# Optimization experiments

Hardware: AMD Instinct MI355X
Metric: run time of the kernel (lower is better)

Reference implementation:

```python
import jax, jax.numpy as jnp
import numpy as np

B, S, NQ, H, HD = 2, 4096, 576, 32, 128
HID = H * HD  # 4096


def setup_inputs() -> dict:
    key = jax.random.key(0)
    ks = jax.random.split(key, 7)
    sc = 0.02
    return {
        "hidden_states": jax.random.normal(ks[0], (B, S, HID), jnp.float32),
        "by_pass_hidden_states": jax.random.normal(ks[1], (B, NQ, HID), jnp.float32),
        "attention_mask": jnp.zeros((B, 1, S, NQ), jnp.float32),
        "Wq": jax.random.normal(ks[2], (HID, HID), jnp.float32) * sc,
        "Wk": jax.random.normal(ks[3], (HID, HID), jnp.float32) * sc,
        "Wv": jax.random.normal(ks[4], (HID, HID), jnp.float32) * sc,
        "Wo": jax.random.normal(ks[5], (HID, HID), jnp.float32) * sc,
    }


def reference(hidden_states, by_pass_hidden_states, attention_mask, Wq, Wk, Wv, Wo):
    b, s, _ = hidden_states.shape
    nq = by_pass_hidden_states.shape[1]
    # projections (nn.Linear applies x @ W.T); reshape to (b, heads, len, head_dim)
    q = (hidden_states @ Wq.T).reshape(b, s, H, HD).transpose(0, 2, 1, 3)
    k = (by_pass_hidden_states @ Wk.T).reshape(b, nq, H, HD).transpose(0, 2, 1, 3)
    v = (by_pass_hidden_states @ Wv.T).reshape(b, nq, H, HD).transpose(0, 2, 1, 3)
    # eager QK^T -> mask -> fp32 softmax -> V
    scores = jnp.einsum("bhsd,bhqd->bhsq", q, k) / jnp.sqrt(jnp.float32(HD))
    scores = scores + attention_mask  # (b,1,s,nq) broadcast over heads
    attn = jax.nn.softmax(scores.astype(jnp.float32), axis=-1).astype(q.dtype)
    out = jnp.einsum("bhsq,bhqd->bhsd", attn, v)
    out = out.transpose(0, 2, 1, 3).reshape(b, s, HID)
    return out @ Wo.T
```

## Files before the change

kernel.cpp:

```cpp
#include <hip/hip_runtime.h>
#include <stdint.h>

#define Bn   2
#define Sn   4096
#define NQn  576
#define Hn   32
#define HDn  128
#define HIDn 4096

typedef unsigned short bfu;
typedef short short8 __attribute__((ext_vector_type(8)));
typedef float f32x4 __attribute__((ext_vector_type(4)));

__device__ __forceinline__ bfu f2b(float f) {
  uint32_t x = __builtin_bit_cast(uint32_t, f);
  return (bfu)((x + 0x7fffu + ((x >> 16) & 1u)) >> 16);
}

__device__ __forceinline__ void gload16(const void* g, void* l) {
  __builtin_amdgcn_global_load_lds(
      (const __attribute__((address_space(1))) uint32_t*)g,
      (__attribute__((address_space(3))) uint32_t*)l, 16, 0, 0);
}

__device__ __forceinline__ void cast8(const float* s, bfu* d, long i) {
  const float4* in4 = (const float4*)s;
  float4 a = in4[2 * i], c = in4[2 * i + 1];
  short8 v;
  v[0] = (short)f2b(a.x); v[1] = (short)f2b(a.y);
  v[2] = (short)f2b(a.z); v[3] = (short)f2b(a.w);
  v[4] = (short)f2b(c.x); v[5] = (short)f2b(c.y);
  v[6] = (short)f2b(c.z); v[7] = (short)f2b(c.w);
  ((short8*)d)[i] = v;
}

__global__ void cast_f32_bf16(const float* __restrict__ in, bfu* __restrict__ out,
                              int n8) {
  long i = (long)blockIdx.x * 256 + threadIdx.x;
  if (i >= n8) return;
  cast8(in, out, i);
}

__global__ void cast5(const float* s0, bfu* d0, int n0, const float* s1, bfu* d1,
                      int n1, const float* s2, bfu* d2, int n2, const float* s3,
                      bfu* d3, int n3, const float* s4, bfu* d4, int n4) {
  long gid = (long)blockIdx.x * 256 + threadIdx.x;
  if (gid < n0) { cast8(s0, d0, gid); return; }
  gid -= n0;
  if (gid < n1) { cast8(s1, d1, gid); return; }
  gid -= n1;
  if (gid < n2) { cast8(s2, d2, gid); return; }
  gid -= n2;
  if (gid < n3) { cast8(s3, d3, gid); return; }
  gid -= n3;
  if (gid < n4) cast8(s4, d4, gid);
}

template <int WRITE_BF16>
__global__ __launch_bounds__(512, 2)
void gemm_bt256(const bfu* __restrict__ A, const bfu* __restrict__ Bm,
                void* __restrict__ Cout, int M, int N, int K) {
  __shared__ __align__(16) bfu Asm[2][256 * 64];
  __shared__ __align__(16) bfu Bsm[2][256 * 64];
  const int tid = threadIdx.x;
  const int wave = tid >> 6, lane = tid & 63;
  const int lr = lane & 15, kq = lane >> 4;
  const int wm = wave >> 2, wn = wave & 3;
  const long m0 = (long)blockIdx.y * 256, n0 = (long)blockIdx.x * 256;
  const int NT = K >> 6;

  const int c0j = tid >> 3, c0c = tid & 7;
  const int c1j = (512 + tid) >> 3, c1c = tid & 7;
  const bfu* aSrc0 = A + (m0 + c0j) * (long)K + ((c0c ^ (c0j & 7)) * 8);
  const bfu* aSrc1 = A + (m0 + c1j) * (long)K + ((c1c ^ (c1j & 7)) * 8);
  const bfu* bSrc0 = Bm + (n0 + c0j) * (long)K + ((c0c ^ (c0j & 7)) * 8);
  const bfu* bSrc1 = Bm + (n0 + c1j) * (long)K + ((c1c ^ (c1j & 7)) * 8);

  auto stageA = [&](int t, int buf, int half) {
    long koff = (long)t * 64 + (long)half * 128 * K;
    gload16(aSrc0 + koff, &Asm[buf][half * 8192 + (wave * 64) * 8]);
    gload16(aSrc1 + koff, &Asm[buf][half * 8192 + (512 + wave * 64) * 8]);
  };
  auto stageB = [&](int t, int buf, int half) {
    long koff = (long)t * 64 + (long)half * 128 * K;
    gload16(bSrc0 + koff, &Bsm[buf][half * 8192 + (wave * 64) * 8]);
    gload16(bSrc1 + koff, &Bsm[buf][half * 8192 + (512 + wave * 64) * 8]);
  };
  auto ldsA = [&](int buf, int mf, int ks) -> short8 {
    int row = (mf >> 2) * 128 + wm * 64 + (mf & 3) * 16 + lr;
    int off = (row * 128 + ks * 64 + kq * 16) ^ ((row & 7) << 4);
    return *(const short8*)((const char*)Asm[buf] + off);
  };
  auto ldsB = [&](int buf, int nf, int ks) -> short8 {
    int row = (nf >> 1) * 128 + wn * 32 + (nf & 1) * 16 + lr;
    int off = (row * 128 + ks * 64 + kq * 16) ^ ((row & 7) << 4);
    return *(const short8*)((const char*)Bsm[buf] + off);
  };

  f32x4 acc[8][4] = {};
  short8 a0[4][2], a1[4][2], b0[2][2], b1[2][2];

#define MFMA16(MB, NB, AA, BB)                                                  \
  _Pragma("unroll") for (int mf = 0; mf < 4; ++mf)                              \
      _Pragma("unroll") for (int ks = 0; ks < 2; ++ks)                          \
      _Pragma("unroll") for (int nf = 0; nf < 2; ++nf)                          \
      acc[MB + mf][NB + nf] = __builtin_amdgcn_mfma_f32_16x16x32_bf16(          \
          AA[mf][ks], BB[nf][ks], acc[MB + mf][NB + nf], 0, 0, 0);

  stageA(0, 0, 0); stageB(0, 0, 0); stageB(0, 0, 1); stageA(0, 0, 1);
  stageA(1, 1, 0); stageB(1, 1, 0); stageB(1, 1, 1); stageA(1, 1, 1);
  asm volatile("s_waitcnt vmcnt(6)" ::: "memory");
  __builtin_amdgcn_s_barrier();

  for (int tp = 0; tp < NT; tp += 2) {
    const bool more = (tp + 2 < NT);
#pragma unroll
    for (int hh = 0; hh < 2; ++hh) {
      const int bb = hh;
      const int ts = tp + hh + 2;
#pragma unroll
      for (int mf = 0; mf < 4; ++mf) {
        a0[mf][0] = ldsA(bb, mf, 0);
        a0[mf][1] = ldsA(bb, mf, 1);
      }
#pragma unroll
      for (int nf = 0; nf < 2; ++nf) {
        b0[nf][0] = ldsB(bb, nf, 0);
        b0[nf][1] = ldsB(bb, nf, 1);
      }
      asm volatile("s_waitcnt lgkmcnt(8)" ::: "memory");
      __builtin_amdgcn_s_barrier();
      asm volatile("s_waitcnt lgkmcnt(0)" ::: "memory");
      __builtin_amdgcn_s_setprio(1);
      MFMA16(0, 0, a0, b0)
      __builtin_amdgcn_s_setprio(0);
      __builtin_amdgcn_s_barrier();
#pragma unroll
      for (int nf = 0; nf < 2; ++nf) {
        b1[nf][0] = ldsB(bb, 2 + nf, 0);
        b1[nf][1] = ldsB(bb, 2 + nf, 1);
      }
      if (more) { stageA(ts, bb, 0); stageB(ts, bb, 0); }
      __builtin_amdgcn_s_barrier();
      asm volatile("s_waitcnt lgkmcnt(0)" ::: "memory");
      __builtin_amdgcn_s_setprio(1);
      MFMA16(0, 2, a0, b1)
      __builtin_amdgcn_s_setprio(0);
      __builtin_amdgcn_s_barrier();
#pragma unroll
      for (int mf = 0; mf < 4; ++mf) {
        a1[mf][0] = ldsA(bb, 4 + mf, 0);
        a1[mf][1] = ldsA(bb, 4 + mf, 1);
      }
      if (more) stageB(ts, bb, 1);
      __builtin_amdgcn_s_barrier();
      asm volatile("s_waitcnt lgkmcnt(0)" ::: "memory");
      __builtin_amdgcn_s_setprio(1);
      MFMA16(4, 2, a1, b1)
      __builtin_amdgcn_s_setprio(0);
      __builtin_amdgcn_s_barrier();
      if (more) stageA(ts, bb, 1);
      __builtin_amdgcn_s_barrier();
      __builtin_amdgcn_s_setprio(1);
      MFMA16(4, 0, a1, b0)
      __builtin_amdgcn_s_setprio(0);
      if (more) {
        asm volatile("s_waitcnt vmcnt(6)" ::: "memory");
      } else if (hh == 0) {
        asm volatile("s_waitcnt vmcnt(0)" ::: "memory");
      }
      __builtin_amdgcn_s_barrier();
    }
  }
#undef MFMA16

#pragma unroll
  for (int mf = 0; mf < 8; ++mf)
#pragma unroll
    for (int nf = 0; nf < 4; ++nf)
#pragma unroll
      for (int r = 0; r < 4; ++r) {
        long row = m0 + (mf >> 2) * 128 + wm * 64 + (mf & 3) * 16 + kq * 4 + r;
        long col = n0 + (nf >> 1) * 128 + wn * 32 + (nf & 1) * 16 + lr;
        float v = acc[mf][nf][r];
        if (WRITE_BF16)
          ((bfu*)Cout)[row * N + col] = f2b(v);
        else
          ((float*)Cout)[row * N + col] = v;
      }
}

template <int WRITE_BF16>
__global__ __launch_bounds__(256, 2)
void gemm_bt(const bfu* __restrict__ A, const bfu* __restrict__ Bm,
             void* __restrict__ Cout, int M, int N, int K) {
  __shared__ __align__(16) bfu As[128 * 32];
  __shared__ __align__(16) bfu Bs[128 * 32];
  const int tid = threadIdx.x;
  const int wave = tid >> 6, lane = tid & 63;
  const int lr = lane & 15, kq = lane >> 4;
  const int wm = wave >> 1, wn = wave & 1;
  const long m0 = (long)blockIdx.y * 128, n0 = (long)blockIdx.x * 128;

  f32x4 acc[4][4] = {};

  for (int kk = 0; kk < K; kk += 32) {
#pragma unroll
    for (int i = 0; i < 2; ++i) {
      int tt = i * 256 + tid;
      long row = tt >> 2;
      int col = (tt & 3) * 8;
      gload16(A + (m0 + row) * K + kk + col, &As[(i * 256 + wave * 64) * 8]);
      gload16(Bm + (n0 + row) * K + kk + col, &Bs[(i * 256 + wave * 64) * 8]);
    }
    __syncthreads();
    short8 a[4], b[4];
#pragma unroll
    for (int mt = 0; mt < 4; ++mt)
      a[mt] = *(const short8*)&As[(wm * 64 + mt * 16 + lr) * 32 + kq * 8];
#pragma unroll
    for (int nt = 0; nt < 4; ++nt)
      b[nt] = *(const short8*)&Bs[(wn * 64 + nt * 16 + lr) * 32 + kq * 8];
#pragma unroll
    for (int mt = 0; mt < 4; ++mt)
#pragma unroll
      for (int nt = 0; nt < 4; ++nt)
        acc[mt][nt] = __builtin_amdgcn_mfma_f32_16x16x32_bf16(
            a[mt], b[nt], acc[mt][nt], 0, 0, 0);
    __syncthreads();
  }
#pragma unroll
  for (int mt = 0; mt < 4; ++mt)
#pragma unroll
    for (int nt = 0; nt < 4; ++nt)
#pragma unroll
      for (int r = 0; r < 4; ++r) {
        long row = m0 + wm * 64 + mt * 16 + kq * 4 + r;
        long col = n0 + wn * 64 + nt * 16 + lr;
        float v = acc[mt][nt][r];
        if (WRITE_BF16)
          ((bfu*)Cout)[row * N + col] = f2b(v);
        else
          ((float*)Cout)[row * N + col] = v;
      }
}

__global__ void transpose_v(const bfu* __restrict__ KVb, bfu* __restrict__ Vt) {
  __shared__ bfu t[32][33];
  const int bh = blockIdx.z;
  const int tq = blockIdx.x;
  const int td = blockIdx.y;
  const int b = bh >> 5, h = bh & 31;
  const int tx = threadIdx.x & 31, ty = threadIdx.x >> 5;
  const bfu* src =
      KVb + ((long)(b * NQn + tq * 32)) * 8192 + 4096 + h * HDn + td * 32;
#pragma unroll
  for (int i = 0; i < 32; i += 8) t[ty + i][tx] = src[(long)(ty + i) * 8192 + tx];
  __syncthreads();
  bfu* dst = Vt + ((long)bh * HDn + td * 32) * NQn + tq * 32;
#pragma unroll
  for (int i = 0; i < 32; i += 8) dst[(long)(ty + i) * NQn + tx] = t[tx][ty + i];
}

__global__ __launch_bounds__(256, 4)
void attn_kernel(const bfu* __restrict__ Qb, const bfu* __restrict__ KVb,
                 const bfu* __restrict__ Vt, const float* __restrict__ mask,
                 bfu* __restrict__ AO) {
  __shared__ __align__(16) bfu Ks[2][4096];
  __shared__ __align__(16) bfu Vs[2][4096];
  const int bid = blockIdx.x;
  const int h = bid & (Hn - 1);
  const int b = (bid >> 5) & (Bn - 1);
  const int qt0 = bid >> 6;
  const long q0 = (long)qt0 * 64;
  const int tid = threadIdx.x;
  const int wave = tid >> 6, lane = tid & 63;
  const int lr = lane & 15, kq = lane >> 4;
  const float scale = 0.08838834764831845f;

  const long qrow = (long)b * Sn + q0 + wave * 16 + lr;
  const bfu* Kblk = KVb + (long)b * NQn * 8192 + h * HDn;
  const bfu* Vblk = Vt + ((long)(b * Hn + h)) * HDn * NQn;
  const float* mrow = mask + ((long)b * Sn + q0 + wave * 16 + lr) * NQn;

  auto stageK = [&](int kt, int buf) {
#pragma unroll
    for (int i = 0; i < 2; ++i) {
      int c = i * 256 + tid;
      int j = c >> 4, c16 = c & 15;
      gload16(Kblk + (long)(kt * 32 + j) * 8192 + ((c16 ^ (j & 7)) * 8),
              &Ks[buf][(i * 256 + wave * 64) * 8]);
    }
  };
  auto stageV = [&](int kt, int buf) {
#pragma unroll
    for (int i = 0; i < 2; ++i) {
      int c = i * 256 + tid;
      int j = c >> 2, c4 = c & 3;
      gload16(Vblk + (long)j * NQn + kt * 32 + c4 * 8,
              &Vs[buf][(i * 256 + wave * 64) * 8]);
    }
  };

  stageK(0, 0);
  stageV(0, 0);

  const bfu* Qbase = Qb + qrow * HIDn + h * HDn;
  short8 qf[4];
#pragma unroll
  for (int ks = 0; ks < 4; ++ks)
    qf[ks] = *(const short8*)&Qbase[ks * 32 + kq * 8];

  f32x4 o[8] = {};
  float rsum = 0.f;

  for (int kt = 0; kt < 18; ++kt) {
    __syncthreads();
    const int buf = kt & 1;
    if (kt < 17) {
      stageK(kt + 1, buf ^ 1);
      stageV(kt + 1, buf ^ 1);
    }
    const char* kb = (const char*)Ks[buf];
    f32x4 s0 = {}, s1 = {};
#pragma unroll
    for (int ks = 0; ks < 4; ++ks) {
      short8 kf0 = *(const short8*)(kb + ((lr * 256 + ks * 64 + kq * 16) ^
                                          ((lr & 7) << 4)));
      short8 kf1 = *(const short8*)(kb + (((16 + lr) * 256 + ks * 64 + kq * 16) ^
                                          ((lr & 7) << 4)));
      s0 = __builtin_amdgcn_mfma_f32_16x16x32_bf16(kf0, qf[ks], s0, 0, 0, 0);
      s1 = __builtin_amdgcn_mfma_f32_16x16x32_bf16(kf1, qf[ks], s1, 0, 0, 0);
    }
    float4 m0 = *(const float4*)&mrow[kt * 32 + kq * 4];
    float4 m1 = *(const float4*)&mrow[kt * 32 + 16 + kq * 4];
    float p00 = __expf(s0[0] * scale + m0.x), p01 = __expf(s0[1] * scale + m0.y);
    float p02 = __expf(s0[2] * scale + m0.z), p03 = __expf(s0[3] * scale + m0.w);
    float p10 = __expf(s1[0] * scale + m1.x), p11 = __expf(s1[1] * scale + m1.y);
    float p12 = __expf(s1[2] * scale + m1.z), p13 = __expf(s1[3] * scale + m1.w);
    rsum += ((p00 + p01) + (p02 + p03)) + ((p10 + p11) + (p12 + p13));
    int pk0_0 = (int)((uint32_t)f2b(p00) | ((uint32_t)f2b(p01) << 16));
    int pk0_1 = (int)((uint32_t)f2b(p02) | ((uint32_t)f2b(p03) << 16));
    int pk1_0 = (int)((uint32_t)f2b(p10) | ((uint32_t)f2b(p11) << 16));
    int pk1_1 = (int)((uint32_t)f2b(p12) | ((uint32_t)f2b(p13) << 16));
    const int sLo = lr + (((kq & 1) << 1) << 4);
    const int sHi = sLo + 16;
    int b0, b1, b2, b3;
    {
      int v0 = __shfl(pk0_0, sLo, 64), v1 = __shfl(pk1_0, sLo, 64);
      b0 = (kq < 2) ? v0 : v1;
      v0 = __shfl(pk0_1, sLo, 64); v1 = __shfl(pk1_1, sLo, 64);
      b1 = (kq < 2) ? v0 : v1;
      v0 = __shfl(pk0_0, sHi, 64); v1 = __shfl(pk1_0, sHi, 64);
      b2 = (kq < 2) ? v0 : v1;
      v0 = __shfl(pk0_1, sHi, 64); v1 = __shfl(pk1_1, sHi, 64);
      b3 = (kq < 2) ? v0 : v1;
    }
    int4 pfi = {b0, b1, b2, b3};
    short8 pfrag = __builtin_bit_cast(short8, pfi);
    const char* vb = (const char*)Vs[buf];
#pragma unroll
    for (int dt = 0; dt < 8; ++dt) {
      short8 vf = *(const short8*)(vb + ((dt * 16 + lr) * 64 + kq * 16));
      o[dt] = __builtin_amdgcn_mfma_f32_16x16x32_bf16(vf, pfrag, o[dt], 0, 0, 0);
    }
  }

  rsum += __shfl_xor(rsum, 16, 64);
  rsum += __shfl_xor(rsum, 32, 64);
  const float inv = 1.0f / rsum;

  bfu* Obase = AO + qrow * HIDn + h * HDn;
#pragma unroll
  for (int dt = 0; dt < 8; ++dt) {
    uint64_t pk = (uint64_t)f2b(o[dt][0] * inv) |
                  ((uint64_t)f2b(o[dt][1] * inv) << 16) |
                  ((uint64_t)f2b(o[dt][2] * inv) << 32) |
                  ((uint64_t)f2b(o[dt][3] * inv) << 48);
    *(uint64_t*)&Obase[dt * 16 + kq * 4] = pk;
  }
}

extern "C" void kernel_launch(void* const* d_in, const int* in_sizes, int n_in,
                              void* d_out, int out_size, void* d_ws, size_t ws_size,
                              hipStream_t stream) {
  const float* hs = (const float*)d_in[0];
  const float* bp = (const float*)d_in[1];
  const float* mask = (const float*)d_in[2];
  const float* Wq = (const float*)d_in[3];
  const float* Wk = (const float*)d_in[4];
  const float* Wv = (const float*)d_in[5];
  const float* Wo = (const float*)d_in[6];
  float* out = (float*)d_out;

  const long M1 = (long)Bn * Sn;
  const long M2 = (long)Bn * NQn;
  char* ws = (char*)d_ws;
  bfu* hb = (bfu*)(ws + 0);
  bfu* bb = (bfu*)(ws + 67108864);
  bfu* w1 = (bfu*)(ws + 76546048);
  bfu* wkv = (bfu*)(ws + 110100480);
  bfu* Qb = (bfu*)(ws + 177209344);
  bfu* KVb = (bfu*)(ws + 244318208);
  bfu* Vt = (bfu*)(ws + 263192576);

  const int n8_hs = (int)(M1 * HIDn / 8);
  const int n8_bp = (int)(M2 * HIDn / 8);
  const int n8_w = (int)((long)HIDn * HIDn / 8);
  const long tot8 = (long)n8_hs + n8_bp + 3L * n8_w;
  cast5<<<dim3((int)(tot8 / 256)), dim3(256), 0, stream>>>(
      hs, hb, n8_hs, bp, bb, n8_bp, Wq, w1, n8_w, Wk, wkv, n8_w, Wv,
      wkv + (long)HIDn * HIDn, n8_w);

  gemm_bt256<1><<<dim3(HIDn / 256, M1 / 256), dim3(512), 0, stream>>>(
      hb, w1, Qb, (int)M1, HIDn, HIDn);
  gemm_bt<1><<<dim3(8192 / 128, M2 / 128), dim3(256), 0, stream>>>(
      bb, wkv, KVb, (int)M2, 8192, HIDn);

  cast_f32_bf16<<<dim3(n8_w / 256), dim3(256), 0, stream>>>(
      Wo, w1, n8_w);
  transpose_v<<<dim3(NQn / 32, HDn / 32, Bn * Hn), dim3(256), 0, stream>>>(
      KVb, Vt);

  attn_kernel<<<dim3((Sn / 64) * Bn * Hn), dim3(256), 0, stream>>>(
      Qb, KVb, Vt, mask, hb );

  gemm_bt256<0><<<dim3(HIDn / 256, M1 / 256), dim3(512), 0, stream>>>(
      hb, w1, out, (int)M1, HIDn, HIDn);
}
```

Before: 889.5 us.

## Double attention query tile to 128 rows per block and fold Wo cast into first cast

```diff
diff --git a/kernel.cpp b/kernel.cpp
--- a/kernel.cpp
+++ b/kernel.cpp
@@ -56,6 +56,24 @@
   if (gid < n4) cast8(s4, d4, gid);
 }
 
+__global__ void cast6(const float* s0, bfu* d0, int n0, const float* s1, bfu* d1,
+                      int n1, const float* s2, bfu* d2, int n2, const float* s3,
+                      bfu* d3, int n3, const float* s4, bfu* d4, int n4,
+                      const float* s5, bfu* d5, int n5) {
+  long gid = (long)blockIdx.x * 256 + threadIdx.x;
+  if (gid < n0) { cast8(s0, d0, gid); return; }
+  gid -= n0;
+  if (gid < n1) { cast8(s1, d1, gid); return; }
+  gid -= n1;
+  if (gid < n2) { cast8(s2, d2, gid); return; }
+  gid -= n2;
+  if (gid < n3) { cast8(s3, d3, gid); return; }
+  gid -= n3;
+  if (gid < n4) { cast8(s4, d4, gid); return; }
+  gid -= n4;
+  if (gid < n5) cast8(s5, d5, gid);
+}
+
 template <int WRITE_BF16>
 __global__ __launch_bounds__(512, 2)
 void gemm_bt256(const bfu* __restrict__ A, const bfu* __restrict__ Bm,
@@ -262,7 +280,7 @@
   for (int i = 0; i < 32; i += 8) dst[(long)(ty + i) * NQn + tx] = t[tx][ty + i];
 }
 
-__global__ __launch_bounds__(256, 4)
+__global__ __launch_bounds__(512, 4)
 void attn_kernel(const bfu* __restrict__ Qb, const bfu* __restrict__ KVb,
                  const bfu* __restrict__ Vt, const float* __restrict__ mask,
                  bfu* __restrict__ AO) {
@@ -272,7 +290,7 @@
   const int h = bid & (Hn - 1);
   const int b = (bid >> 5) & (Bn - 1);
   const int qt0 = bid >> 6;
-  const long q0 = (long)qt0 * 64;
+  const long q0 = (long)qt0 * 128;
   const int tid = threadIdx.x;
   const int wave = tid >> 6, lane = tid & 63;
   const int lr = lane & 15, kq = lane >> 4;
@@ -281,25 +299,17 @@
   const long qrow = (long)b * Sn + q0 + wave * 16 + lr;
   const bfu* Kblk = KVb + (long)b * NQn * 8192 + h * HDn;
   const bfu* Vblk = Vt + ((long)(b * Hn + h)) * HDn * NQn;
-  const float* mrow = mask + ((long)b * Sn + q0 + wave * 16 + lr) * NQn;
+  const float* mrow = mask + qrow * NQn;
 
   auto stageK = [&](int kt, int buf) {
-#pragma unroll
-    for (int i = 0; i < 2; ++i) {
-      int c = i * 256 + tid;
-      int j = c >> 4, c16 = c & 15;
-      gload16(Kblk + (long)(kt * 32 + j) * 8192 + ((c16 ^ (j & 7)) * 8),
-              &Ks[buf][(i * 256 + wave * 64) * 8]);
-    }
+    int j = tid >> 4, c16 = tid & 15;
+    gload16(Kblk + (long)(kt * 32 + j) * 8192 + ((c16 ^ (j & 7)) * 8),
+            &Ks[buf][(wave * 64) * 8]);
   };
   auto stageV = [&](int kt, int buf) {
-#pragma unroll
-    for (int i = 0; i < 2; ++i) {
-      int c = i * 256 + tid;
-      int j = c >> 2, c4 = c & 3;
-      gload16(Vblk + (long)j * NQn + kt * 32 + c4 * 8,
-              &Vs[buf][(i * 256 + wave * 64) * 8]);
-    }
+    int j = tid >> 2, c4 = tid & 3;
+    gload16(Vblk + (long)j * NQn + kt * 32 + c4 * 8,
+            &Vs[buf][(wave * 64) * 8]);
   };
 
   stageK(0, 0);
@@ -403,28 +413,40 @@
   bfu* Qb = (bfu*)(ws + 177209344);
   bfu* KVb = (bfu*)(ws + 244318208);
   bfu* Vt = (bfu*)(ws + 263192576);
+  const bool bigws = (ws_size >= 306184192);
+  bfu* wo = bigws ? (bfu*)(ws + 272629760) : w1;
 
   const int n8_hs = (int)(M1 * HIDn / 8);
   const int n8_bp = (int)(M2 * HIDn / 8);
   const int n8_w = (int)((long)HIDn * HIDn / 8);
-  const long tot8 = (long)n8_hs + n8_bp + 3L * n8_w;
-  cast5<<<dim3((int)(tot8 / 256)), dim3(256), 0, stream>>>(
-      hs, hb, n8_hs, bp, bb, n8_bp, Wq, w1, n8_w, Wk, wkv, n8_w, Wv,
-      wkv + (long)HIDn * HIDn, n8_w);
+
+  if (bigws) {
+    const long tot8 = (long)n8_hs + n8_bp + 4L * n8_w;
+    cast6<<<dim3((int)(tot8 / 256)), dim3(256), 0, stream>>>(
+        hs, hb, n8_hs, bp, bb, n8_bp, Wq, w1, n8_w, Wk, wkv, n8_w, Wv,
+        wkv + (long)HIDn * HIDn, n8_w, Wo, wo, n8_w);
+  } else {
+    const long tot8 = (long)n8_hs + n8_bp + 3L * n8_w;
+    cast5<<<dim3((int)(tot8 / 256)), dim3(256), 0, stream>>>(
+        hs, hb, n8_hs, bp, bb, n8_bp, Wq, w1, n8_w, Wk, wkv, n8_w, Wv,
+        wkv + (long)HIDn * HIDn, n8_w);
+  }
 
   gemm_bt256<1><<<dim3(HIDn / 256, M1 / 256), dim3(512), 0, stream>>>(
       hb, w1, Qb, (int)M1, HIDn, HIDn);
   gemm_bt<1><<<dim3(8192 / 128, M2 / 128), dim3(256), 0, stream>>>(
       bb, wkv, KVb, (int)M2, 8192, HIDn);
 
-  cast_f32_bf16<<<dim3(n8_w / 256), dim3(256), 0, stream>>>(
-      Wo, w1, n8_w);
+  if (!bigws) {
+    cast_f32_bf16<<<dim3(n8_w / 256), dim3(256), 0, stream>>>(
+        Wo, w1, n8_w);
+  }
   transpose_v<<<dim3(NQn / 32, HDn / 32, Bn * Hn), dim3(256), 0, stream>>>(
       KVb, Vt);
 
-  attn_kernel<<<dim3((Sn / 64) * Bn * Hn), dim3(256), 0, stream>>>(
+  attn_kernel<<<dim3((Sn / 128) * Bn * Hn), dim3(512), 0, stream>>>(
       Qb, KVb, Vt, mask, hb );
 
   gemm_bt256<0><<<dim3(HIDn / 256, M1 / 256), dim3(512), 0, stream>>>(
-      hb, w1, out, (int)M1, HIDn, HIDn);
-}
+      hb, wo, out, (int)M1, HIDn, HIDn);
+}
```

Result: slower. 934.7 us (+5.1%).
